# Optimization experiments

Hardware: AMD Instinct MI355X
Metric: run time of the kernel (lower is better)

## Reference

```python
import jax, jax.numpy as jnp
import numpy as np

NUM_MODELS = 16
NUM_CLASSES = 17929
HIDDEN = 4
BATCH = 512


def setup_inputs() -> dict:
    key = jax.random.key(0)
    k1, k2, k3, k4, k5 = jax.random.split(key, 5)
    x = jax.random.normal(k1, (NUM_MODELS, BATCH, NUM_CLASSES), dtype=jnp.float32)
    # stacked per-class Linear(num_models, hidden) weights/biases
    W1 = jax.random.normal(k2, (NUM_CLASSES, HIDDEN, NUM_MODELS), dtype=jnp.float32) * 0.1
    b1 = jax.random.normal(k3, (NUM_CLASSES, HIDDEN), dtype=jnp.float32) * 0.1
    # stacked per-class Linear(hidden, 1) weights (squeezed) / biases
    W2 = jax.random.normal(k4, (NUM_CLASSES, HIDDEN), dtype=jnp.float32) * 0.1
    b2 = jax.random.normal(k5, (NUM_CLASSES,), dtype=jnp.float32) * 0.1
    return {"x": x, "W1": W1, "b1": b1, "W2": W2, "b2": b2}


def reference(x, W1, b1, W2, b2):
    # x: [M, B, C] -> permute(1, 2, 0) -> [B, C, M]
    xp = jnp.transpose(x, (1, 2, 0))
    # per-class first Linear + ReLU: h[b,c,h] = relu(sum_m xp[b,c,m] * W1[c,h,m] + b1[c,h])
    h = jax.nn.relu(jnp.einsum('bcm,chm->bch', xp, W1) + b1[None, :, :])
    # per-class second Linear(hidden -> 1), concatenated over classes -> [B, C]
    out = jnp.einsum('bch,ch->bc', h, W2) + b2[None, :]
    return out
```

## Files before the change

kernel.cpp:

```cpp
#include <hip/hip_runtime.h>


#define NUM_MODELS 16
#define HIDDEN 4
#define BATCH 512
#define NUM_CLASSES 17929
#define KB 16
#define CT 256

__global__ __launch_bounds__(CT) void FamilyMLPLinear_kernel(
    const float* __restrict__ x,
    const float* __restrict__ W1,
    const float* __restrict__ b1,
    const float* __restrict__ W2,
    const float* __restrict__ b2,
    float* __restrict__ out)
{
    const int c = blockIdx.x * CT + threadIdx.x;
    if (c >= NUM_CLASSES) return;
    const int b0 = blockIdx.y * KB;

    float w1[HIDDEN][NUM_MODELS];
    const float4* W1v = (const float4*)(W1 + (size_t)c * (HIDDEN * NUM_MODELS));
    #pragma unroll
    for (int j = 0; j < HIDDEN; ++j) {
        #pragma unroll
        for (int q = 0; q < NUM_MODELS / 4; ++q) {
            float4 v = W1v[j * (NUM_MODELS / 4) + q];
            w1[j][q * 4 + 0] = v.x;
            w1[j][q * 4 + 1] = v.y;
            w1[j][q * 4 + 2] = v.z;
            w1[j][q * 4 + 3] = v.w;
        }
    }
    const float4 b1v = *(const float4*)(b1 + (size_t)c * HIDDEN);
    const float bias1[HIDDEN] = {b1v.x, b1v.y, b1v.z, b1v.w};
    const float4 w2v = *(const float4*)(W2 + (size_t)c * HIDDEN);
    const float w2[HIDDEN] = {w2v.x, w2v.y, w2v.z, w2v.w};
    const float bias2 = b2[c];

    const size_t BC = (size_t)BATCH * NUM_CLASSES;

    #pragma unroll 1
    for (int bi = 0; bi < KB; ++bi) {
        const int b = b0 + bi;
        const float* xp = x + (size_t)b * NUM_CLASSES + c;

        float xv[NUM_MODELS];
        #pragma unroll
        for (int m = 0; m < NUM_MODELS; ++m)
            xv[m] = xp[(size_t)m * BC];

        float acc = bias2;
        #pragma unroll
        for (int j = 0; j < HIDDEN; ++j) {
            float h = bias1[j];
            #pragma unroll
            for (int m = 0; m < NUM_MODELS; ++m)
                h = fmaf(xv[m], w1[j][m], h);
            h = fmaxf(h, 0.0f);
            acc = fmaf(h, w2[j], acc);
        }
        out[(size_t)b * NUM_CLASSES + c] = acc;
    }
}

extern "C" void kernel_launch(void* const* d_in, const int* in_sizes, int n_in,
                              void* d_out, int out_size, void* d_ws, size_t ws_size,
                              hipStream_t stream) {
    const float* x  = (const float*)d_in[0];
    const float* W1 = (const float*)d_in[1];
    const float* b1 = (const float*)d_in[2];
    const float* W2 = (const float*)d_in[3];
    const float* b2 = (const float*)d_in[4];
    float* out = (float*)d_out;

    dim3 grid((NUM_CLASSES + CT - 1) / CT, BATCH / KB);
    FamilyMLPLinear_kernel<<<grid, CT, 0, stream>>>(x, W1, b1, W2, b2, out);
}
```

Before: 772.5 us.

## Stage x rows into LDS via aligned global_load_lds with nontemporal stores

Full tiles now copy the 16 model rows for each batch element into shared memory with 16-byte direct-to-LDS loads. The start address is rounded down to 4-float alignment, because the rows are misaligned when the class count is odd. Threads then read their values from LDS, and the few shifted past the tile end fall back to global loads. Output uses nontemporal stores, and the partial tail tile keeps the old scalar path. This replaces scalar 4-byte loads with wide loads, but each batch step adds two block barriers and serializes the load with the compute.

```diff
diff --git a/kernel.cpp b/kernel.cpp
--- a/kernel.cpp
+++ b/kernel.cpp
@@ -8,6 +8,9 @@
 #define KB 16
 #define CT 256
 
+typedef __attribute__((address_space(1))) const void as1_void;
+typedef __attribute__((address_space(3))) void as3_void;
+
 __global__ __launch_bounds__(CT) void FamilyMLPLinear_kernel(
     const float* __restrict__ x,
     const float* __restrict__ W1,
@@ -16,12 +19,16 @@
     const float* __restrict__ b2,
     float* __restrict__ out)
 {
-    const int c = blockIdx.x * CT + threadIdx.x;
-    if (c >= NUM_CLASSES) return;
+    __shared__ float xs[NUM_MODELS][CT];
+
+    const int t  = threadIdx.x;
+    const int c0 = blockIdx.x * CT;
     const int b0 = blockIdx.y * KB;
+    const int c  = c0 + t;
+    const int cw = (c < NUM_CLASSES) ? c : (NUM_CLASSES - 1);
 
     float w1[HIDDEN][NUM_MODELS];
-    const float4* W1v = (const float4*)(W1 + (size_t)c * (HIDDEN * NUM_MODELS));
+    const float4* W1v = (const float4*)(W1 + (size_t)cw * (HIDDEN * NUM_MODELS));
     #pragma unroll
     for (int j = 0; j < HIDDEN; ++j) {
         #pragma unroll
@@ -33,35 +40,81 @@
             w1[j][q * 4 + 3] = v.w;
         }
     }
-    const float4 b1v = *(const float4*)(b1 + (size_t)c * HIDDEN);
+    const float4 b1v = *(const float4*)(b1 + (size_t)cw * HIDDEN);
     const float bias1[HIDDEN] = {b1v.x, b1v.y, b1v.z, b1v.w};
-    const float4 w2v = *(const float4*)(W2 + (size_t)c * HIDDEN);
+    const float4 w2v = *(const float4*)(W2 + (size_t)cw * HIDDEN);
     const float w2[HIDDEN] = {w2v.x, w2v.y, w2v.z, w2v.w};
-    const float bias2 = b2[c];
+    const float bias2 = b2[cw];
 
     const size_t BC = (size_t)BATCH * NUM_CLASSES;
 
-    #pragma unroll 1
-    for (int bi = 0; bi < KB; ++bi) {
-        const int b = b0 + bi;
-        const float* xp = x + (size_t)b * NUM_CLASSES + c;
+    if (c0 + CT <= NUM_CLASSES) {
+        const int lane = t & 63;
+        const int wv   = t >> 6;
 
-        float xv[NUM_MODELS];
-        #pragma unroll
-        for (int m = 0; m < NUM_MODELS; ++m)
-            xv[m] = xp[(size_t)m * BC];
+        #pragma unroll 1
+        for (int bi = 0; bi < KB; ++bi) {
+            const int b = b0 + bi;
+            const size_t row0 = (size_t)b * NUM_CLASSES + c0;
+            const int   sb  = (int)(row0 & 3);
+            const size_t A0 = row0 - (size_t)sb;
 
-        float acc = bias2;
-        #pragma unroll
-        for (int j = 0; j < HIDDEN; ++j) {
-            float h = bias1[j];
             #pragma unroll
-            for (int m = 0; m < NUM_MODELS; ++m)
-                h = fmaf(xv[m], w1[j][m], h);
-            h = fmaxf(h, 0.0f);
-            acc = fmaf(h, w2[j], acc);
+            for (int r = 0; r < 4; ++r) {
+                const int m = wv * 4 + r;
+                const float* gp = x + (size_t)m * BC + A0 + (size_t)(lane << 2);
+                __builtin_amdgcn_global_load_lds((as1_void*)gp, (as3_void*)&xs[m][0],
+                                                 16, 0, 0);
+            }
+            __syncthreads();
+
+            float xv[NUM_MODELS];
+            const int ti = t + sb;
+            if (ti < CT) {
+                #pragma unroll
+                for (int m = 0; m < NUM_MODELS; ++m) xv[m] = xs[m][ti];
+            } else {
+                const float* xp = x + row0 + t;
+                #pragma unroll
+                for (int m = 0; m < NUM_MODELS; ++m) xv[m] = xp[(size_t)m * BC];
+            }
+
+            float acc = bias2;
+            #pragma unroll
+            for (int j = 0; j < HIDDEN; ++j) {
+                float h = bias1[j];
+                #pragma unroll
+                for (int m = 0; m < NUM_MODELS; ++m)
+                    h = fmaf(xv[m], w1[j][m], h);
+                h = fmaxf(h, 0.0f);
+                acc = fmaf(h, w2[j], acc);
+            }
+            __builtin_nontemporal_store(acc, out + (size_t)b * NUM_CLASSES + c);
+            __syncthreads();
         }
-        out[(size_t)b * NUM_CLASSES + c] = acc;
+    } else {
+        if (c < NUM_CLASSES) {
+            #pragma unroll 1
+            for (int bi = 0; bi < KB; ++bi) {
+                const int b = b0 + bi;
+                const float* xp = x + (size_t)b * NUM_CLASSES + c;
+                float xv[NUM_MODELS];
+                #pragma unroll
+                for (int m = 0; m < NUM_MODELS; ++m)
+                    xv[m] = xp[(size_t)m * BC];
+                float acc = bias2;
+                #pragma unroll
+                for (int j = 0; j < HIDDEN; ++j) {
+                    float h = bias1[j];
+                    #pragma unroll
+                    for (int m = 0; m < NUM_MODELS; ++m)
+                        h = fmaf(xv[m], w1[j][m], h);
+                    h = fmaxf(h, 0.0f);
+                    acc = fmaf(h, w2[j], acc);
+                }
+                out[(size_t)b * NUM_CLASSES + c] = acc;
+            }
+        }
     }
 }
 
```

Measured after the change: 812.1 us. 5.1% more time.
